# Optimization experiments

Hardware: AMD Instinct MI355X
Metric: run time of the kernel (lower is better)

Reference implementation:

```python
import jax, jax.numpy as jnp
import numpy as np

GN_EPS = 1e-5
NUM_GROUPS = 32


def setup_inputs() -> dict:
    key = jax.random.key(0)
    ks = jax.random.split(key, 4)
    B, K, N = 8192, 2048, 4096
    bound = 1.0 / np.sqrt(K)
    return {
        "x": jax.random.normal(ks[0], (B, K), dtype=jnp.float32),
        "weight": jax.random.normal(ks[1], (N, K), dtype=jnp.float32) * bound,
        "bias_lin": jax.random.uniform(ks[2], (N,), dtype=jnp.float32, minval=-bound, maxval=bound),
        "bias_extra": jax.random.normal(ks[3], (N,), dtype=jnp.float32),
        "gn_weight": jnp.ones((N,), dtype=jnp.float32),
        "gn_bias": jnp.zeros((N,), dtype=jnp.float32),
    }


def reference(x, weight, bias_lin, bias_extra, gn_weight, gn_bias):
    # Fused GEMM + bias + Swish + extra bias:  y = swish(x @ W.T + b_lin) + b_ex
    z = jnp.einsum("bk,nk->bn", x, weight) + bias_lin          # [B, N]
    y = z * jax.nn.sigmoid(z) + bias_extra                      # Swish + extra bias
    # GroupNorm over channel groups
    B, N = y.shape
    G = NUM_GROUPS
    yg = y.reshape(B, G, N // G)
    mean = jnp.mean(yg, axis=2, keepdims=True)
    var = jnp.mean(jnp.square(yg - mean), axis=2, keepdims=True)  # biased variance
    y_norm = ((yg - mean) * jax.lax.rsqrt(var + GN_EPS)).reshape(B, N)
    return y_norm * gn_weight + gn_bias
```

## Files before the change

### kernel.cpp

```cpp
#include <hip/hip_runtime.h>


typedef __attribute__((ext_vector_type(8))) short short8;
typedef __attribute__((ext_vector_type(4))) float f32x4;

#define M_DIM 8192
#define N_DIM 4096
#define K_DIM 2048
#define BM 128
#define BN 128
#define BK 32
#define NT (K_DIM / BK)

#define AS1 __attribute__((address_space(1)))
#define AS3 __attribute__((address_space(3)))

__global__ void f32_to_bf16_k(const float* __restrict__ in, ushort* __restrict__ out, int n8) {
    int i = blockIdx.x * blockDim.x + threadIdx.x;
    if (i >= n8) return;
    const float4* p = (const float4*)in + 2 * (size_t)i;
    float4 a = p[0], b = p[1];
    float v[8] = {a.x, a.y, a.z, a.w, b.x, b.y, b.z, b.w};
    ushort rr[8];
#pragma unroll
    for (int j = 0; j < 8; ++j) {
        unsigned u = __float_as_uint(v[j]);
        rr[j] = (ushort)((u + 0x7fffu + ((u >> 16) & 1u)) >> 16);
    }
    uint4 o;
    o.x = (unsigned)rr[0] | ((unsigned)rr[1] << 16);
    o.y = (unsigned)rr[2] | ((unsigned)rr[3] << 16);
    o.z = (unsigned)rr[4] | ((unsigned)rr[5] << 16);
    o.w = (unsigned)rr[6] | ((unsigned)rr[7] << 16);
    ((uint4*)out)[i] = o;
}


#define BAR() __builtin_amdgcn_s_barrier()
#define LGKM0() do { asm volatile("s_waitcnt lgkmcnt(0)" ::: "memory"); __builtin_amdgcn_sched_barrier(0); } while (0)
#define VMC(n_) do { asm volatile("s_waitcnt vmcnt(" #n_ ")" ::: "memory"); __builtin_amdgcn_sched_barrier(0); } while (0)

__global__ __launch_bounds__(256, 3) void gemm_swish_gn(
    const ushort* __restrict__ xb, const ushort* __restrict__ wb,
    const float* __restrict__ bias_lin, const float* __restrict__ bias_extra,
    const float* __restrict__ gn_w, const float* __restrict__ gn_b,
    float* __restrict__ out)
{
    extern __shared__ __align__(16) ushort lds[];

    const int t = threadIdx.x;
    const int w = t >> 6;
    const int l = t & 63;
    const int wm = w >> 1;
    const int wn = w & 1;
    const int h = l >> 4;
    const int r = l & 15;

    const int bid = blockIdx.x;
    const int xcd = bid & 7;
    const int pp = bid >> 3;
    const int brow = (xcd & 3) * 16 + (pp & 15);
    const int bcol = (xcd >> 2) * 16 + (pp >> 4);

    const int srow = t >> 2;
    const int sslot = (t & 3) ^ ((t >> 3) & 3);
    const ushort* pA0 = xb + (size_t)(brow * BM + srow) * K_DIM + sslot * 8;
    const ushort* pA1 = pA0 + (size_t)64 * K_DIM;
    const ushort* pB0 = wb + (size_t)(bcol * BN + srow) * K_DIM + sslot * 8;
    const ushort* pB1 = pB0 + (size_t)64 * K_DIM;
    const int dst = t * 8;

#define STG(P_) do {                                                           \
    __builtin_amdgcn_global_load_lds((const AS1 void*)pA0,                     \
        (AS3 void*)&lds[(P_) * 8192 + dst], 16, 0, 0);                         \
    __builtin_amdgcn_global_load_lds((const AS1 void*)pA1,                     \
        (AS3 void*)&lds[(P_) * 8192 + 2048 + dst], 16, 0, 0);                  \
    __builtin_amdgcn_global_load_lds((const AS1 void*)pB0,                     \
        (AS3 void*)&lds[(P_) * 8192 + 4096 + dst], 16, 0, 0);                  \
    __builtin_amdgcn_global_load_lds((const AS1 void*)pB1,                     \
        (AS3 void*)&lds[(P_) * 8192 + 6144 + dst], 16, 0, 0);                  \
    pA0 += BK; pA1 += BK; pB0 += BK; pB1 += BK; } while (0)

    const int slotR = (h ^ ((r >> 1) & 3)) << 3;
    const int aOff = (wm * 64 + r) * 32 + slotR;
    const int bOff = 4096 + (wn * 64 + r) * 32 + slotR;

    f32x4 acc[4][4];
#pragma unroll
    for (int m = 0; m < 4; ++m)
#pragma unroll
        for (int n = 0; n < 4; ++n)
            acc[m][n] = f32x4{0.f, 0.f, 0.f, 0.f};

    STG(0);
    STG(1);
    VMC(4);
    BAR();

    short8 aF[4], bF[4];

#define PH(P_, PN_, T_)                                                        \
  {                                                                            \
    _Pragma("unroll") for (int m = 0; m < 4; ++m)                              \
        aF[m] = *(const short8*)&lds[(P_) * 8192 + aOff + m * 512];            \
    _Pragma("unroll") for (int n = 0; n < 4; ++n)                              \
        bF[n] = *(const short8*)&lds[(P_) * 8192 + bOff + n * 512];            \
    if ((T_) < NT - 2) { STG(PN_); }                                           \
    if ((T_) >= NT - 2) { VMC(0); } else { VMC(4); }                           \
    BAR(); LGKM0();                                                            \
    __builtin_amdgcn_s_setprio(1);                                             \
    _Pragma("unroll") for (int m = 0; m < 4; ++m)                              \
        _Pragma("unroll") for (int n = 0; n < 4; ++n)                          \
            acc[m][n] = __builtin_amdgcn_mfma_f32_16x16x32_bf16(               \
                aF[m], bF[n], acc[m][n], 0, 0, 0);                             \
    __builtin_amdgcn_s_setprio(0);                                             \
  }

#pragma unroll 1
    for (int tb = 0; tb < NT - 1; tb += 3) {
        PH(0, 2, tb);
        PH(1, 0, tb + 1);
        PH(2, 1, tb + 2);
    }
    PH(0, 2, NT - 1);

    const int colbase = bcol * BN + wn * 64;
    float bl[4], be[4], gwv[4], gbv[4];
#pragma unroll
    for (int n = 0; n < 4; ++n) {
        int col = colbase + n * 16 + r;
        bl[n] = bias_lin[col];
        be[n] = bias_extra[col];
        gwv[n] = gn_w[col];
        gbv[n] = gn_b[col];
    }

    float s1[4][4], s2[4][4];
#pragma unroll
    for (int m = 0; m < 4; ++m)
#pragma unroll
        for (int j = 0; j < 4; ++j) { s1[m][j] = 0.f; s2[m][j] = 0.f; }

#pragma unroll
    for (int m = 0; m < 4; ++m)
#pragma unroll
        for (int n = 0; n < 4; ++n)
#pragma unroll
            for (int j = 0; j < 4; ++j) {
                float z = acc[m][n][j] + bl[n];
                float sw = z / (1.f + __expf(-z)) + be[n];
                acc[m][n][j] = sw;
                s1[m][j] += sw;
                s2[m][j] += sw * sw;
            }

#pragma unroll
    for (int mask = 1; mask < 16; mask <<= 1) {
#pragma unroll
        for (int m = 0; m < 4; ++m)
#pragma unroll
            for (int j = 0; j < 4; ++j) {
                s1[m][j] += __shfl_xor(s1[m][j], mask, 16);
                s2[m][j] += __shfl_xor(s2[m][j], mask, 16);
            }
    }

    float* sred = (float*)&lds[24576];
    if (r == 0) {
#pragma unroll
        for (int m = 0; m < 4; ++m)
#pragma unroll
            for (int j = 0; j < 4; ++j) {
                int row = wm * 64 + m * 16 + h * 4 + j;
                sred[(0 * 2 + wn) * 128 + row] = s1[m][j];
                sred[(1 * 2 + wn) * 128 + row] = s2[m][j];
            }
    }
    __syncthreads();

    const size_t orow0 = (size_t)brow * BM;
#pragma unroll
    for (int m = 0; m < 4; ++m)
#pragma unroll
        for (int j = 0; j < 4; ++j) {
            int row = wm * 64 + m * 16 + h * 4 + j;
            float mu = (sred[0 * 128 + row] + sred[1 * 128 + row]) * (1.f / 128.f);
            float ex2 = (sred[2 * 128 + row] + sred[3 * 128 + row]) * (1.f / 128.f);
            float var = ex2 - mu * mu;
            float rs = rsqrtf(var + 1e-5f);
            float* orow = out + (orow0 + row) * N_DIM;
#pragma unroll
            for (int n = 0; n < 4; ++n) {
                int col = colbase + n * 16 + r;
                orow[col] = (acc[m][n][j] - mu) * rs * gwv[n] + gbv[n];
            }
        }
}

extern "C" void kernel_launch(void* const* d_in, const int* in_sizes, int n_in,
                              void* d_out, int out_size, void* d_ws, size_t ws_size,
                              hipStream_t stream) {
    const float* x        = (const float*)d_in[0];
    const float* weight   = (const float*)d_in[1];
    const float* bias_lin = (const float*)d_in[2];
    const float* bias_ex  = (const float*)d_in[3];
    const float* gn_w     = (const float*)d_in[4];
    const float* gn_b     = (const float*)d_in[5];
    float* out = (float*)d_out;

    ushort* xb = (ushort*)d_ws;
    ushort* wb = xb + (size_t)M_DIM * K_DIM;

    {
        int n8 = (M_DIM * K_DIM) / 8;
        f32_to_bf16_k<<<n8 / 256, 256, 0, stream>>>(x, xb, n8);
    }
    {
        int n8 = (N_DIM * K_DIM) / 8;
        f32_to_bf16_k<<<n8 / 256, 256, 0, stream>>>(weight, wb, n8);
    }

    const size_t ldsB = 3 * 8192 * sizeof(ushort) + 2048 * sizeof(float);
    dim3 grid((M_DIM / BM) * (N_DIM / BN));
    gemm_swish_gn<<<grid, 256, ldsB, stream>>>(xb, wb, bias_lin, bias_ex, gn_w, gn_b, out);
}
```

Before: 215.7 us.

## Replace triple-buffered BK=32 pipeline with single-buffer BK=64 synchronous loop

Doubles the K tile to 64 and drops the three-stage LDS ring with manual vmcnt/barrier scheduling. Each iteration now issues the loads, waits at a full __syncthreads, computes, and syncs again. This halves the iteration count, cuts LDS use to one buffer and uses a new XOR swizzle for 64-wide rows. The cost is that global-to-LDS loads no longer overlap with MFMA work, so latency is exposed on every K step.

New measurement: 182.0 us. -15.6%, faster.

```diff
diff --git a/kernel.cpp b/kernel.cpp
--- a/kernel.cpp
+++ b/kernel.cpp
@@ -9,7 +9,7 @@
 #define K_DIM 2048
 #define BM 128
 #define BN 128
-#define BK 32
+#define BK 64
 #define NT (K_DIM / BK)
 
 #define AS1 __attribute__((address_space(1)))
@@ -36,10 +36,6 @@
 }
 
 
-#define BAR() __builtin_amdgcn_s_barrier()
-#define LGKM0() do { asm volatile("s_waitcnt lgkmcnt(0)" ::: "memory"); __builtin_amdgcn_sched_barrier(0); } while (0)
-#define VMC(n_) do { asm volatile("s_waitcnt vmcnt(" #n_ ")" ::: "memory"); __builtin_amdgcn_sched_barrier(0); } while (0)
-
 __global__ __launch_bounds__(256, 3) void gemm_swish_gn(
     const ushort* __restrict__ xb, const ushort* __restrict__ wb,
     const float* __restrict__ bias_lin, const float* __restrict__ bias_extra,
@@ -62,28 +58,24 @@
     const int brow = (xcd & 3) * 16 + (pp & 15);
     const int bcol = (xcd >> 2) * 16 + (pp >> 4);
 
-    const int srow = t >> 2;
-    const int sslot = (t & 3) ^ ((t >> 3) & 3);
-    const ushort* pA0 = xb + (size_t)(brow * BM + srow) * K_DIM + sslot * 8;
-    const ushort* pA1 = pA0 + (size_t)64 * K_DIM;
-    const ushort* pB0 = wb + (size_t)(bcol * BN + srow) * K_DIM + sslot * 8;
-    const ushort* pB1 = pB0 + (size_t)64 * K_DIM;
+    const int s = t >> 3;
+    const int scol = (((t & 7) ^ (s & 7)) << 3);
+    const ushort* pA = xb + (size_t)(brow * BM + s) * K_DIM + scol;
+    const ushort* pB = wb + (size_t)(bcol * BN + s) * K_DIM + scol;
     const int dst = t * 8;
 
-#define STG(P_) do {                                                           \
-    __builtin_amdgcn_global_load_lds((const AS1 void*)pA0,                     \
-        (AS3 void*)&lds[(P_) * 8192 + dst], 16, 0, 0);                         \
-    __builtin_amdgcn_global_load_lds((const AS1 void*)pA1,                     \
-        (AS3 void*)&lds[(P_) * 8192 + 2048 + dst], 16, 0, 0);                  \
-    __builtin_amdgcn_global_load_lds((const AS1 void*)pB0,                     \
-        (AS3 void*)&lds[(P_) * 8192 + 4096 + dst], 16, 0, 0);                  \
-    __builtin_amdgcn_global_load_lds((const AS1 void*)pB1,                     \
-        (AS3 void*)&lds[(P_) * 8192 + 6144 + dst], 16, 0, 0);                  \
-    pA0 += BK; pA1 += BK; pB0 += BK; pB1 += BK; } while (0)
-
-    const int slotR = (h ^ ((r >> 1) & 3)) << 3;
-    const int aOff = (wm * 64 + r) * 32 + slotR;
-    const int bOff = 4096 + (wn * 64 + r) * 32 + slotR;
+#define STG_A(ROFF) __builtin_amdgcn_global_load_lds(                          \
+        (const AS1 void*)(pA + (size_t)(ROFF) * K_DIM),                        \
+        (AS3 void*)&lds[(ROFF) * 64 + dst], 16, 0, 0)
+#define STG_B(ROFF) __builtin_amdgcn_global_load_lds(                          \
+        (const AS1 void*)(pB + (size_t)(ROFF) * K_DIM),                        \
+        (AS3 void*)&lds[8192 + (ROFF) * 64 + dst], 16, 0, 0)
+
+    const int xr8 = (r & 7) << 3;
+    const int aOff0 = (wm * 64 + r) * 64 + ((h << 3) ^ xr8);
+    const int aOff1 = aOff0 ^ 32;
+    const int bOff0 = 8192 + (wn * 64 + r) * 64 + ((h << 3) ^ xr8);
+    const int bOff1 = bOff0 ^ 32;
 
     f32x4 acc[4][4];
 #pragma unroll
@@ -92,37 +84,36 @@
         for (int n = 0; n < 4; ++n)
             acc[m][n] = f32x4{0.f, 0.f, 0.f, 0.f};
 
-    STG(0);
-    STG(1);
-    VMC(4);
-    BAR();
-
-    short8 aF[4], bF[4];
-
-#define PH(P_, PN_, T_)                                                        \
-  {                                                                            \
-    _Pragma("unroll") for (int m = 0; m < 4; ++m)                              \
-        aF[m] = *(const short8*)&lds[(P_) * 8192 + aOff + m * 512];            \
-    _Pragma("unroll") for (int n = 0; n < 4; ++n)                              \
-        bF[n] = *(const short8*)&lds[(P_) * 8192 + bOff + n * 512];            \
-    if ((T_) < NT - 2) { STG(PN_); }                                           \
-    if ((T_) >= NT - 2) { VMC(0); } else { VMC(4); }                           \
-    BAR(); LGKM0();                                                            \
-    __builtin_amdgcn_s_setprio(1);                                             \
-    _Pragma("unroll") for (int m = 0; m < 4; ++m)                              \
-        _Pragma("unroll") for (int n = 0; n < 4; ++n)                          \
-            acc[m][n] = __builtin_amdgcn_mfma_f32_16x16x32_bf16(               \
-                aF[m], bF[n], acc[m][n], 0, 0, 0);                             \
-    __builtin_amdgcn_s_setprio(0);                                             \
-  }
+    short8 aF[4][2], bF[4][2];
 
 #pragma unroll 1
-    for (int tb = 0; tb < NT - 1; tb += 3) {
-        PH(0, 2, tb);
-        PH(1, 0, tb + 1);
-        PH(2, 1, tb + 2);
-    }
-    PH(0, 2, NT - 1);
+    for (int kt = 0; kt < NT; ++kt) {
+        STG_A(0); STG_A(32); STG_A(64); STG_A(96);
+        STG_B(0); STG_B(32); STG_B(64); STG_B(96);
+        pA += BK; pB += BK;
+        __syncthreads();
+
+#pragma unroll
+        for (int m = 0; m < 4; ++m) {
+            aF[m][0] = *(const short8*)&lds[aOff0 + m * 1024];
+            aF[m][1] = *(const short8*)&lds[aOff1 + m * 1024];
+        }
+#pragma unroll
+        for (int n = 0; n < 4; ++n) {
+            bF[n][0] = *(const short8*)&lds[bOff0 + n * 1024];
+            bF[n][1] = *(const short8*)&lds[bOff1 + n * 1024];
+        }
+#pragma unroll
+        for (int kk = 0; kk < 2; ++kk)
+#pragma unroll
+            for (int m = 0; m < 4; ++m)
+#pragma unroll
+                for (int n = 0; n < 4; ++n)
+                    acc[m][n] = __builtin_amdgcn_mfma_f32_16x16x32_bf16(
+                        aF[m][kk], bF[n][kk], acc[m][n], 0, 0, 0);
+
+        __syncthreads();
+    }
 
     const int colbase = bcol * BN + wn * 64;
     float bl[4], be[4], gwv[4], gbv[4];
@@ -165,7 +156,7 @@
             }
     }
 
-    float* sred = (float*)&lds[24576];
+    float* sred = (float*)&lds[16384];
     if (r == 0) {
 #pragma unroll
         for (int m = 0; m < 4; ++m)
@@ -220,7 +211,7 @@
         f32_to_bf16_k<<<n8 / 256, 256, 0, stream>>>(weight, wb, n8);
     }
 
-    const size_t ldsB = 3 * 8192 * sizeof(ushort) + 2048 * sizeof(float);
+    const size_t ldsB = 16384 * sizeof(ushort) + 512 * sizeof(float);
     dim3 grid((M_DIM / BM) * (N_DIM / BN));
     gemm_swish_gn<<<grid, 256, ldsB, stream>>>(xb, wb, bias_lin, bias_ex, gn_w, gn_b, out);
 }
```
